# Optimization experiments

Hardware: AMD Instinct MI355X
Metric: run time of the kernel (lower is better)

The kernel has to match this reference:

```python
import jax, jax.numpy as jnp
import numpy as np
from itertools import combinations

N_QUBITS = 8
N_TRASH = 2
N_LAYERS = 4
BATCH = 32768
DIM = 2 ** N_QUBITS  # 256


def _cz_pairs():
    # same CZ pattern as layer() in the torch module; all pairs are distinct,
    # and CZ gates are diagonal and commute, so they fuse into one sign mask.
    pairs = list(combinations(range(N_TRASH), 2))
    for idx in range(N_TRASH):
        for i in range(N_TRASH):
            for j in range(N_TRASH + i, N_QUBITS, N_TRASH):
                pairs.append(((idx + i) % N_TRASH, j))
    return pairs


def _cz_layer_sign():
    bits = np.indices((2,) * N_QUBITS)  # [n_qubits, 2,...,2]; wire 0 = MSB (PennyLane order)
    sign = np.ones((2,) * N_QUBITS, np.float32)
    for a, b in _cz_pairs():
        sign = sign * (1.0 - 2.0 * (bits[a] * bits[b]).astype(np.float32))
    return jnp.asarray(sign)[None]  # broadcast over batch

_CZ_SIGN = _cz_layer_sign()


def _ry(state, theta, w):
    # RY(theta) on wire w, batched over leading axis. state: [B,2,...,2] complex64
    c = jnp.cos(theta / 2).astype(jnp.complex64)
    s = jnp.sin(theta / 2).astype(jnp.complex64)
    g = jnp.stack([jnp.stack([c, -s]), jnp.stack([s, c])])  # [2,2]
    out = jnp.tensordot(g, state, axes=((1,), (1 + w,)))
    return jnp.moveaxis(out, 0, 1 + w)


def _axis_vec(vals, w):
    shape = [1] * (N_QUBITS + 1)
    shape[1 + w] = 2
    return jnp.asarray(vals, dtype=jnp.complex64).reshape(shape)


def _apply_pauli(state, w, p):
    if p == 'X':
        return jnp.flip(state, axis=1 + w)
    if p == 'Y':
        return jnp.flip(state, axis=1 + w) * _axis_vec([-1j, 1j], w)
    return state * _axis_vec([1.0 + 0j, -1.0 + 0j], w)  # Z


def _forward(x, weights):
    # AmplitudeEmbedding(normalize=True)
    norm = jnp.sqrt(jnp.sum(x * x, axis=-1, keepdims=True))
    psi = (x / norm).astype(jnp.complex64).reshape((-1,) + (2,) * N_QUBITS)
    for l in range(N_LAYERS - 1):
        for q in range(N_QUBITS):
            psi = _ry(psi, weights[l * N_QUBITS + q], q)
        psi = psi * _CZ_SIGN  # all CZs of the layer fused into one diagonal
    base = (N_LAYERS - 1) * N_QUBITS
    for q in range(N_TRASH):  # last_layer: RY on trash qubits only
        psi = _ry(psi, weights[base + q], q)

    axes = tuple(range(1, N_QUBITS + 1))
    conj_psi = jnp.conj(psi)

    def ev(op_state):
        return jnp.sum(conj_psi * op_state, axis=axes).real.astype(jnp.float32)

    w0, w1 = 6, 7
    terms = [
        ev(_apply_pauli(psi, w0, 'X')),
        ev(_apply_pauli(psi, w0, 'Y')),
        ev(_apply_pauli(psi, w0, 'Z')),
        ev(_apply_pauli(psi, w1, 'X')),
        ev(_apply_pauli(psi, w1, 'Y')),
        ev(_apply_pauli(psi, w1, 'Z')),
        ev(_apply_pauli(_apply_pauli(psi, w0, 'X'), w1, 'X')),
        ev(_apply_pauli(_apply_pauli(psi, w0, 'Y'), w1, 'Y')),
        ev(_apply_pauli(_apply_pauli(psi, w0, 'Z'), w1, 'Z')),
    ]
    return jnp.stack(terms, axis=1)  # [B, 9]


def setup_inputs() -> dict:
    key = jax.random.key(0)
    kx, kw = jax.random.split(key)
    x = jax.random.normal(kx, (BATCH, DIM), dtype=jnp.float32)
    n_w = N_LAYERS * N_QUBITS - (N_QUBITS - N_TRASH)  # 26
    weights = jax.random.normal(kw, (n_w,), dtype=jnp.float32)
    return {'x': x, 'weights': weights}


def reference(x, weights):
    return _forward(x, weights)
```

## Files before the change

kernel.cpp:

```cpp
#include <hip/hip_runtime.h>
#include <math.h>

#define DIM 256
typedef float v2f __attribute__((ext_vector_type(2)));

__device__ __forceinline__ v2f mk2(float a, float b) { v2f r; r.x = a; r.y = b; return r; }

__device__ __forceinline__ float rl(float v, int l) {
    return __uint_as_float(__builtin_amdgcn_readlane(__float_as_uint(v), l));
}

template<int B2>
__device__ __forceinline__ void ry_pk(v2f* v, float c, float s) {
#pragma unroll
    for (int p = 0; p < 16; ++p)
        if (!(p & (1 << B2))) {
            const int q = p | (1 << B2);
            v2f lo = v[p], hi = v[q];
            v[p] = c * lo - s * hi;
            v[q] = s * lo + c * hi;
        }
}

__device__ __forceinline__ void ry_intra(v2f* v, float c, float s) {
#pragma unroll
    for (int p = 0; p < 16; ++p) {
        float lo = v[p].x, hi = v[p].y;
        v[p].x = fmaf(-s, hi, c * lo);
        v[p].y = fmaf(s, lo, c * hi);
    }
}

__global__ __launch_bounds__(256) void qae_kernel(const float* __restrict__ x,
                                                  const float* __restrict__ w,
                                                  float* __restrict__ out,
                                                  int batch) {
    __shared__ float4 lds4[2048];
    const int lane = threadIdx.x & 63;
    const int wave = blockIdx.x * 4 + (threadIdx.x >> 6);
    const int l3   = lane & 7;
    const int e    = lane >> 3;
    const int eb   = wave * 8 + e;
    float4* W = lds4 + (threadIdx.x >> 6) * 512 + e * 64;

    float h = 0.f;
    if (lane < 20) h = 0.5f * w[lane < 18 ? lane : lane + 4];
    const float cv = __cosf(h), sv = __sinf(h);
#define RYP(B2, slot) ry_pk<B2>(v, rl(cv, slot), rl(sv, slot))
#define RYI(slot)     ry_intra(v, rl(cv, slot), rl(sv, slot))

    const int a0 = (l3 >> 2) & 1, a1 = (l3 >> 1) & 1, a2 = l3 & 1;
    const int aa = a0 & a1, dd = a0 ^ a1;
    const float fE = (aa ^ (dd & a2)) ? -1.f : 1.f;
    const float fO = ((aa ^ (dd & a2)) ^ dd) ? -1.f : 1.f;
    const float pB = (__popc(l3) & 1) ? -1.f : 1.f;
    const v2f mA0 = mk2(fE, fO), mA1 = mk2(fO, fE);
    const v2f mBp = mk2(pB, -pB);

    v2f v[16];
    if (eb < batch) {
        const float* xp = x + (size_t)eb * DIM + l3 * 4;
#pragma unroll
        for (int u = 0; u < 8; ++u) {
            float4 f = *(const float4*)(xp + u * 32);
            v[2 * u]     = mk2(f.x, f.y);
            v[2 * u + 1] = mk2(f.z, f.w);
        }
    } else {
#pragma unroll
        for (int p = 0; p < 16; ++p) v[p] = mk2(0.f, 0.f);
    }
    float nrm2 = 0.f;
#pragma unroll
    for (int p = 0; p < 16; ++p) nrm2 += v[p].x * v[p].x + v[p].y * v[p].y;

    RYP(3, 0); RYP(2, 1); RYP(1, 2);

#pragma unroll
    for (int g = 0; g < 8; ++g)
        W[g * 8 + (l3 ^ g)] = make_float4(v[2*g].x, v[2*g].y, v[2*g+1].x, v[2*g+1].y);
#pragma unroll
    for (int k = 0; k < 8; ++k) {
        float4 f = W[l3 * 8 + (k ^ l3)];
        v[2 * k] = mk2(f.x, f.y); v[2 * k + 1] = mk2(f.z, f.w);
    }

    RYP(3, 3); RYP(2, 4); RYP(1, 5); RYP(0, 6); RYI(7);
#pragma unroll
    for (int p = 0; p < 16; ++p) v[p] *= (__popc(p) & 1) ? mA1 : mA0;
    RYP(3, 11); RYP(2, 12); RYP(1, 13); RYP(0, 14); RYI(15);

#pragma unroll
    for (int k = 0; k < 8; ++k)
        W[l3 * 8 + (k ^ l3)] = make_float4(v[2*k].x, v[2*k].y, v[2*k+1].x, v[2*k+1].y);
#pragma unroll
    for (int g = 0; g < 8; ++g) {
        float4 f = W[g * 8 + (l3 ^ g)];
        v[2 * g] = mk2(f.x, f.y); v[2 * g + 1] = mk2(f.z, f.w);
    }

    RYP(3, 8); RYP(2, 9); RYP(1, 10);
#pragma unroll
    for (int p = 0; p < 16; ++p) {
        const int w0 = (p >> 3) & 1, w1 = (p >> 2) & 1;
        if (w0 & w1)      v[p] = -v[p];
        else if (w0 ^ w1) v[p] *= (__popc(p & 3) & 1) ? -mBp : mBp;
    }
    RYP(3, 16); RYP(2, 17); RYP(0, 18); RYI(19);
#pragma unroll
    for (int p = 0; p < 16; ++p) {
        const int w0 = (p >> 3) & 1, w1 = (p >> 2) & 1;
        if (w0 & w1)      v[p] = -v[p];
        else if (w0 ^ w1) v[p] *= (__popc(p & 3) & 1) ? -mBp : mBp;
    }
#undef RYP
#undef RYI

    float X6 = 0, X7 = 0, XX = 0, YY = 0, Z6 = 0, Z7 = 0, ZZ = 0;
#pragma unroll
    for (int g = 0; g < 8; ++g) {
        float q0 = v[2*g].x, q1 = v[2*g].y, q2 = v[2*g+1].x, q3 = v[2*g+1].y;
        X6 += q0 * q2 + q1 * q3;
        X7 += q0 * q1 + q2 * q3;
        XX += q0 * q3 + q1 * q2;
        YY += q1 * q2 - q0 * q3;
        float s0 = q0*q0, s1 = q1*q1, s2 = q2*q2, s3 = q3*q3;
        Z6 += s0 + s1 - s2 - s3;
        Z7 += s0 - s1 + s2 - s3;
        ZZ += s0 - s1 - s2 + s3;
    }
    X6 *= 2.f; X7 *= 2.f; XX *= 2.f; YY *= 2.f;

#pragma unroll
    for (int m = 1; m < 8; m <<= 1) {
        nrm2 += __shfl_xor(nrm2, m);
        X6 += __shfl_xor(X6, m);  X7 += __shfl_xor(X7, m);
        XX += __shfl_xor(XX, m);  YY += __shfl_xor(YY, m);
        Z6 += __shfl_xor(Z6, m);  Z7 += __shfl_xor(Z7, m);
        ZZ += __shfl_xor(ZZ, m);
    }

    if (eb < batch) {
        const float inv = 1.f / nrm2;
        float* o = out + (size_t)eb * 9;
        const int t = l3;
        if (t < 7) {
            float val = (t == 0) ? X6 : (t == 1) ? Z6 : (t == 2) ? X7
                      : (t == 3) ? Z7 : (t == 4) ? XX : (t == 5) ? YY : ZZ;
            int off = t + (t >= 1 ? 1 : 0) + (t >= 3 ? 1 : 0);
            o[off] = val * inv;
        } else {
            o[1] = 0.f;
            o[4] = 0.f;
        }
    }
}

extern "C" void kernel_launch(void* const* d_in, const int* in_sizes, int n_in,
                              void* d_out, int out_size, void* d_ws, size_t ws_size,
                              hipStream_t stream) {
    const float* x = (const float*)d_in[0];
    const float* w = (const float*)d_in[1];
    float* out = (float*)d_out;
    const int batch = in_sizes[0] / DIM;

    const int waves  = (batch + 7) / 8;
    const int blocks = (waves + 3) / 4;
    qae_kernel<<<blocks, 256, 0, stream>>>(x, w, out, batch);
}
```

Baseline: 79.62 us.

## Split each state vector over 16 lanes with padded scalar LDS transposes

Each batch element's 256-amplitude state is now spread over 16 lanes holding 16 amplitudes each, down from 8 lanes holding 32, so each wave handles 4 elements instead of 8. The qubit-to-lane mapping and gate ordering are rearranged to match, LDS exchanges use padded scalar strides in place of XOR swizzled float4, and the norm is folded into the final reduction. A launch-bounds occupancy hint is added. This cuts register pressure and raises parallelism, at the cost of twice as many waves, more shuffle steps and scalar LDS traffic.

```diff
diff --git a/kernel.cpp b/kernel.cpp
--- a/kernel.cpp
+++ b/kernel.cpp
@@ -13,7 +13,7 @@
 template<int B2>
 __device__ __forceinline__ void ry_pk(v2f* v, float c, float s) {
 #pragma unroll
-    for (int p = 0; p < 16; ++p)
+    for (int p = 0; p < 8; ++p)
         if (!(p & (1 << B2))) {
             const int q = p | (1 << B2);
             v2f lo = v[p], hi = v[q];
@@ -24,24 +24,27 @@
 
 __device__ __forceinline__ void ry_intra(v2f* v, float c, float s) {
 #pragma unroll
-    for (int p = 0; p < 16; ++p) {
+    for (int p = 0; p < 8; ++p) {
         float lo = v[p].x, hi = v[p].y;
         v[p].x = fmaf(-s, hi, c * lo);
         v[p].y = fmaf(s, lo, c * hi);
     }
 }
 
-__global__ __launch_bounds__(256) void qae_kernel(const float* __restrict__ x,
-                                                  const float* __restrict__ w,
-                                                  float* __restrict__ out,
-                                                  int batch) {
-    __shared__ float4 lds4[2048];
+__global__ __launch_bounds__(256, 6) void qae_kernel(const float* __restrict__ x,
+                                                     const float* __restrict__ w,
+                                                     float* __restrict__ out,
+                                                     int batch) {
+    __shared__ float lds[4 * 4 * 272];
     const int lane = threadIdx.x & 63;
-    const int wave = blockIdx.x * 4 + (threadIdx.x >> 6);
-    const int l3   = lane & 7;
-    const int e    = lane >> 3;
-    const int eb   = wave * 8 + e;
-    float4* W = lds4 + (threadIdx.x >> 6) * 512 + e * 64;
+    const int wid  = threadIdx.x >> 6;
+    const int wave = blockIdx.x * 4 + wid;
+    const int nib  = lane & 15;
+    const int e    = lane >> 4;
+    const int eb   = wave * 4 + e;
+    float* WB = lds + wid * 1088 + e * 272;
+    float* pB = WB + nib * 4;
+    float* pA = WB + (nib >> 2) * 68 + (nib & 3);
 
     float h = 0.f;
     if (lane < 20) h = 0.5f * w[lane < 18 ? lane : lane + 4];
@@ -49,91 +52,86 @@
 #define RYP(B2, slot) ry_pk<B2>(v, rl(cv, slot), rl(sv, slot))
 #define RYI(slot)     ry_intra(v, rl(cv, slot), rl(sv, slot))
 
-    const int a0 = (l3 >> 2) & 1, a1 = (l3 >> 1) & 1, a2 = l3 & 1;
-    const int aa = a0 & a1, dd = a0 ^ a1;
-    const float fE = (aa ^ (dd & a2)) ? -1.f : 1.f;
-    const float fO = ((aa ^ (dd & a2)) ^ dd) ? -1.f : 1.f;
-    const float pB = (__popc(l3) & 1) ? -1.f : 1.f;
-    const v2f mA0 = mk2(fE, fO), mA1 = mk2(fO, fE);
-    const v2f mBp = mk2(pB, -pB);
+    float gE, gO;
+    {
+        const int w0 = (nib >> 3) & 1, w1 = (nib >> 2) & 1;
+        const float s0 = (__popc(nib & 3) & 1) ? -1.f : 1.f;
+        if (w0 & w1)      { gE = -1.f; gO = -1.f; }
+        else if (w0 ^ w1) { gE = s0;   gO = -s0;  }
+        else              { gE = 1.f;  gO = 1.f;  }
+    }
+    const v2f mAe = mk2(gE, gO), mAo = mk2(gO, gE);
+    const float pL = (__popc(nib) & 1) ? -1.f : 1.f;
+    const v2f mBx0 = mk2(pL, -pL), mBx1 = mk2(-pL, pL);
 
-    v2f v[16];
+    v2f v[8];
     if (eb < batch) {
-        const float* xp = x + (size_t)eb * DIM + l3 * 4;
+        const float* xp = x + (size_t)eb * DIM + nib * 4;
 #pragma unroll
-        for (int u = 0; u < 8; ++u) {
-            float4 f = *(const float4*)(xp + u * 32);
+        for (int u = 0; u < 4; ++u) {
+            float4 f = *(const float4*)(xp + u * 64);
             v[2 * u]     = mk2(f.x, f.y);
             v[2 * u + 1] = mk2(f.z, f.w);
         }
     } else {
 #pragma unroll
-        for (int p = 0; p < 16; ++p) v[p] = mk2(0.f, 0.f);
+        for (int p = 0; p < 8; ++p) v[p] = mk2(0.f, 0.f);
     }
-    float nrm2 = 0.f;
-#pragma unroll
-    for (int p = 0; p < 16; ++p) nrm2 += v[p].x * v[p].x + v[p].y * v[p].y;
 
-    RYP(3, 0); RYP(2, 1); RYP(1, 2);
+    RYP(2, 0); RYP(1, 1); RYP(0, 6); RYI(7);
 
 #pragma unroll
-    for (int g = 0; g < 8; ++g)
-        W[g * 8 + (l3 ^ g)] = make_float4(v[2*g].x, v[2*g].y, v[2*g+1].x, v[2*g+1].y);
+    for (int u = 0; u < 4; ++u)
+        *(float4*)(pB + u * 68) = make_float4(v[2*u].x, v[2*u].y, v[2*u+1].x, v[2*u+1].y);
 #pragma unroll
-    for (int k = 0; k < 8; ++k) {
-        float4 f = W[l3 * 8 + (k ^ l3)];
-        v[2 * k] = mk2(f.x, f.y); v[2 * k + 1] = mk2(f.z, f.w);
+    for (int p = 0; p < 8; ++p) {
+        v[p].x = pA[p * 8];
+        v[p].y = pA[p * 8 + 4];
     }
 
-    RYP(3, 3); RYP(2, 4); RYP(1, 5); RYP(0, 6); RYI(7);
+    RYP(2, 2); RYP(1, 3); RYP(0, 4); RYI(5);
 #pragma unroll
-    for (int p = 0; p < 16; ++p) v[p] *= (__popc(p) & 1) ? mA1 : mA0;
-    RYP(3, 11); RYP(2, 12); RYP(1, 13); RYP(0, 14); RYI(15);
+    for (int p = 0; p < 8; ++p) v[p] *= (__popc(p) & 1) ? mAo : mAe;
+    RYP(2, 10); RYP(1, 11); RYP(0, 12); RYI(13);
 
 #pragma unroll
-    for (int k = 0; k < 8; ++k)
-        W[l3 * 8 + (k ^ l3)] = make_float4(v[2*k].x, v[2*k].y, v[2*k+1].x, v[2*k+1].y);
+    for (int p = 0; p < 8; ++p) {
+        pA[p * 8]     = v[p].x;
+        pA[p * 8 + 4] = v[p].y;
+    }
 #pragma unroll
-    for (int g = 0; g < 8; ++g) {
-        float4 f = W[g * 8 + (l3 ^ g)];
-        v[2 * g] = mk2(f.x, f.y); v[2 * g + 1] = mk2(f.z, f.w);
+    for (int u = 0; u < 4; ++u) {
+        float4 f = *(const float4*)(pB + u * 68);
+        v[2 * u] = mk2(f.x, f.y); v[2 * u + 1] = mk2(f.z, f.w);
     }
 
-    RYP(3, 8); RYP(2, 9); RYP(1, 10);
-#pragma unroll
-    for (int p = 0; p < 16; ++p) {
-        const int w0 = (p >> 3) & 1, w1 = (p >> 2) & 1;
-        if (w0 & w1)      v[p] = -v[p];
-        else if (w0 ^ w1) v[p] *= (__popc(p & 3) & 1) ? -mBp : mBp;
-    }
-    RYP(3, 16); RYP(2, 17); RYP(0, 18); RYI(19);
-#pragma unroll
-    for (int p = 0; p < 16; ++p) {
-        const int w0 = (p >> 3) & 1, w1 = (p >> 2) & 1;
-        if (w0 & w1)      v[p] = -v[p];
-        else if (w0 ^ w1) v[p] *= (__popc(p & 3) & 1) ? -mBp : mBp;
-    }
+    RYP(2, 8); RYP(1, 9); RYP(0, 14); RYI(15);
+    v[2] *= mBx0; v[3] *= mBx1; v[4] *= mBx0; v[5] *= mBx1; v[6] = -v[6]; v[7] = -v[7];
+    RYP(2, 16); RYP(1, 17); RYP(0, 18); RYI(19);
+    v[2] *= mBx0; v[3] *= mBx1; v[4] *= mBx0; v[5] *= mBx1; v[6] = -v[6]; v[7] = -v[7];
 #undef RYP
 #undef RYI
 
-    float X6 = 0, X7 = 0, XX = 0, YY = 0, Z6 = 0, Z7 = 0, ZZ = 0;
+    float X6 = 0, X7 = 0, XX = 0, YY = 0, Z6 = 0, Z7 = 0, ZZ = 0, N = 0;
 #pragma unroll
-    for (int g = 0; g < 8; ++g) {
-        float q0 = v[2*g].x, q1 = v[2*g].y, q2 = v[2*g+1].x, q3 = v[2*g+1].y;
+    for (int u = 0; u < 4; ++u) {
+        float q0 = v[2*u].x, q1 = v[2*u].y, q2 = v[2*u+1].x, q3 = v[2*u+1].y;
         X6 += q0 * q2 + q1 * q3;
         X7 += q0 * q1 + q2 * q3;
         XX += q0 * q3 + q1 * q2;
         YY += q1 * q2 - q0 * q3;
-        float s0 = q0*q0, s1 = q1*q1, s2 = q2*q2, s3 = q3*q3;
-        Z6 += s0 + s1 - s2 - s3;
-        Z7 += s0 - s1 + s2 - s3;
-        ZZ += s0 - s1 - s2 + s3;
+        float t01p = q0*q0 + q1*q1, t01m = q0*q0 - q1*q1;
+        float t23p = q2*q2 + q3*q3, t23m = q2*q2 - q3*q3;
+        N  += t01p + t23p;
+        Z6 += t01p - t23p;
+        Z7 += t01m + t23m;
+        ZZ += t01m - t23m;
     }
     X6 *= 2.f; X7 *= 2.f; XX *= 2.f; YY *= 2.f;
 
 #pragma unroll
-    for (int m = 1; m < 8; m <<= 1) {
-        nrm2 += __shfl_xor(nrm2, m);
+    for (int m = 1; m < 16; m <<= 1) {
+        N  += __shfl_xor(N, m);
         X6 += __shfl_xor(X6, m);  X7 += __shfl_xor(X7, m);
         XX += __shfl_xor(XX, m);  YY += __shfl_xor(YY, m);
         Z6 += __shfl_xor(Z6, m);  Z7 += __shfl_xor(Z7, m);
@@ -141,15 +139,15 @@
     }
 
     if (eb < batch) {
-        const float inv = 1.f / nrm2;
+        const float inv = 1.f / N;
         float* o = out + (size_t)eb * 9;
-        const int t = l3;
+        const int t = nib;
         if (t < 7) {
             float val = (t == 0) ? X6 : (t == 1) ? Z6 : (t == 2) ? X7
                       : (t == 3) ? Z7 : (t == 4) ? XX : (t == 5) ? YY : ZZ;
             int off = t + (t >= 1 ? 1 : 0) + (t >= 3 ? 1 : 0);
             o[off] = val * inv;
-        } else {
+        } else if (t == 7) {
             o[1] = 0.f;
             o[4] = 0.f;
         }
@@ -164,7 +162,7 @@
     float* out = (float*)d_out;
     const int batch = in_sizes[0] / DIM;
 
-    const int waves  = (batch + 7) / 8;
+    const int waves  = (batch + 3) / 4;
     const int blocks = (waves + 3) / 4;
     qae_kernel<<<blocks, 256, 0, stream>>>(x, w, out, batch);
 }
```

Result: no change. 78.89 us (-0.9%).

## Precompute circuit unitary and apply it via fp16 MFMA GEMM

Applied to the files above, without the earlier changes.

Splits the work into two kernels. The first builds the full 256x256 circuit unitary by simulating the gates on basis vectors and stores it in fp16, in an MFMA-friendly layout, in the workspace. The second multiplies each batch of input states by this unitary with 16x16x32 fp16 MFMA instructions and reduces the Pauli expectations from the accumulators. This replaces per-sample VALU gate simulation with tensor-core matrix multiplication, at the cost of fp16 rounding of inputs and the unitary, plus repeated staging of U into LDS in every block.

```diff
diff --git a/kernel.cpp b/kernel.cpp
--- a/kernel.cpp
+++ b/kernel.cpp
@@ -2,10 +2,11 @@
 #include <math.h>
 
 #define DIM 256
-typedef float v2f __attribute__((ext_vector_type(2)));
+typedef float v2f  __attribute__((ext_vector_type(2)));
+typedef _Float16 f16x8 __attribute__((ext_vector_type(8)));
+typedef float f32x4 __attribute__((ext_vector_type(4)));
 
 __device__ __forceinline__ v2f mk2(float a, float b) { v2f r; r.x = a; r.y = b; return r; }
-
 __device__ __forceinline__ float rl(float v, int l) {
     return __uint_as_float(__builtin_amdgcn_readlane(__float_as_uint(v), l));
 }
@@ -21,7 +22,6 @@
             v[q] = s * lo + c * hi;
         }
 }
-
 __device__ __forceinline__ void ry_intra(v2f* v, float c, float s) {
 #pragma unroll
     for (int p = 0; p < 16; ++p) {
@@ -31,17 +31,16 @@
     }
 }
 
-__global__ __launch_bounds__(256) void qae_kernel(const float* __restrict__ x,
-                                                  const float* __restrict__ w,
-                                                  float* __restrict__ out,
-                                                  int batch) {
+__global__ __launch_bounds__(256) void qae_buildU(const float* __restrict__ w,
+                                                  _Float16* __restrict__ uf) {
     __shared__ float4 lds4[2048];
     const int lane = threadIdx.x & 63;
-    const int wave = blockIdx.x * 4 + (threadIdx.x >> 6);
+    const int wid  = threadIdx.x >> 6;
+    const int wave = blockIdx.x * 4 + wid;
     const int l3   = lane & 7;
     const int e    = lane >> 3;
-    const int eb   = wave * 8 + e;
-    float4* W = lds4 + (threadIdx.x >> 6) * 512 + e * 64;
+    const int col  = wave * 8 + e;
+    float4* W = lds4 + wid * 512 + e * 64;
 
     float h = 0.f;
     if (lane < 20) h = 0.5f * w[lane < 18 ? lane : lane + 4];
@@ -58,101 +57,135 @@
     const v2f mBp = mk2(pB, -pB);
 
     v2f v[16];
-    if (eb < batch) {
-        const float* xp = x + (size_t)eb * DIM + l3 * 4;
-#pragma unroll
-        for (int u = 0; u < 8; ++u) {
-            float4 f = *(const float4*)(xp + u * 32);
-            v[2 * u]     = mk2(f.x, f.y);
-            v[2 * u + 1] = mk2(f.z, f.w);
-        }
-    } else {
-#pragma unroll
-        for (int p = 0; p < 16; ++p) v[p] = mk2(0.f, 0.f);
-    }
-    float nrm2 = 0.f;
-#pragma unroll
-    for (int p = 0; p < 16; ++p) nrm2 += v[p].x * v[p].x + v[p].y * v[p].y;
+#pragma unroll
+    for (int p = 0; p < 16; ++p) v[p] = mk2(0.f, 0.f);
+    if (((col >> 2) & 7) == l3) {
+        const int p = 2 * (col >> 5) + ((col >> 1) & 1);
+        if (col & 1) v[p].y = 1.f; else v[p].x = 1.f;
+    }
 
     RYP(3, 0); RYP(2, 1); RYP(1, 2);
-
 #pragma unroll
     for (int g = 0; g < 8; ++g)
         W[g * 8 + (l3 ^ g)] = make_float4(v[2*g].x, v[2*g].y, v[2*g+1].x, v[2*g+1].y);
 #pragma unroll
     for (int k = 0; k < 8; ++k) {
         float4 f = W[l3 * 8 + (k ^ l3)];
-        v[2 * k] = mk2(f.x, f.y); v[2 * k + 1] = mk2(f.z, f.w);
-    }
-
+        v[2*k] = mk2(f.x, f.y); v[2*k+1] = mk2(f.z, f.w);
+    }
     RYP(3, 3); RYP(2, 4); RYP(1, 5); RYP(0, 6); RYI(7);
 #pragma unroll
     for (int p = 0; p < 16; ++p) v[p] *= (__popc(p) & 1) ? mA1 : mA0;
     RYP(3, 11); RYP(2, 12); RYP(1, 13); RYP(0, 14); RYI(15);
-
 #pragma unroll
     for (int k = 0; k < 8; ++k)
         W[l3 * 8 + (k ^ l3)] = make_float4(v[2*k].x, v[2*k].y, v[2*k+1].x, v[2*k+1].y);
 #pragma unroll
     for (int g = 0; g < 8; ++g) {
         float4 f = W[g * 8 + (l3 ^ g)];
-        v[2 * g] = mk2(f.x, f.y); v[2 * g + 1] = mk2(f.z, f.w);
-    }
-
+        v[2*g] = mk2(f.x, f.y); v[2*g+1] = mk2(f.z, f.w);
+    }
     RYP(3, 8); RYP(2, 9); RYP(1, 10);
 #pragma unroll
     for (int p = 0; p < 16; ++p) {
-        const int w0 = (p >> 3) & 1, w1 = (p >> 2) & 1;
-        if (w0 & w1)      v[p] = -v[p];
-        else if (w0 ^ w1) v[p] *= (__popc(p & 3) & 1) ? -mBp : mBp;
+        const int b0 = (p >> 3) & 1, b1 = (p >> 2) & 1;
+        if (b0 & b1)      v[p] = -v[p];
+        else if (b0 ^ b1) v[p] *= (__popc(p & 3) & 1) ? -mBp : mBp;
     }
     RYP(3, 16); RYP(2, 17); RYP(0, 18); RYI(19);
 #pragma unroll
     for (int p = 0; p < 16; ++p) {
-        const int w0 = (p >> 3) & 1, w1 = (p >> 2) & 1;
-        if (w0 & w1)      v[p] = -v[p];
-        else if (w0 ^ w1) v[p] *= (__popc(p & 3) & 1) ? -mBp : mBp;
+        const int b0 = (p >> 3) & 1, b1 = (p >> 2) & 1;
+        if (b0 & b1)      v[p] = -v[p];
+        else if (b0 ^ b1) v[p] *= (__popc(p & 3) & 1) ? -mBp : mBp;
     }
 #undef RYP
 #undef RYI
 
-    float X6 = 0, X7 = 0, XX = 0, YY = 0, Z6 = 0, Z7 = 0, ZZ = 0;
-#pragma unroll
-    for (int g = 0; g < 8; ++g) {
-        float q0 = v[2*g].x, q1 = v[2*g].y, q2 = v[2*g+1].x, q3 = v[2*g+1].y;
-        X6 += q0 * q2 + q1 * q3;
-        X7 += q0 * q1 + q2 * q3;
-        XX += q0 * q3 + q1 * q2;
-        YY += q1 * q2 - q0 * q3;
-        float s0 = q0*q0, s1 = q1*q1, s2 = q2*q2, s3 = q3*q3;
-        Z6 += s0 + s1 - s2 - s3;
-        Z7 += s0 - s1 + s2 - s3;
-        ZZ += s0 - s1 - s2 + s3;
-    }
-    X6 *= 2.f; X7 *= 2.f; XX *= 2.f; YY *= 2.f;
-
-#pragma unroll
-    for (int m = 1; m < 8; m <<= 1) {
-        nrm2 += __shfl_xor(nrm2, m);
-        X6 += __shfl_xor(X6, m);  X7 += __shfl_xor(X7, m);
-        XX += __shfl_xor(XX, m);  YY += __shfl_xor(YY, m);
-        Z6 += __shfl_xor(Z6, m);  Z7 += __shfl_xor(Z7, m);
-        ZZ += __shfl_xor(ZZ, m);
-    }
-
-    if (eb < batch) {
-        const float inv = 1.f / nrm2;
-        float* o = out + (size_t)eb * 9;
-        const int t = l3;
-        if (t < 7) {
-            float val = (t == 0) ? X6 : (t == 1) ? Z6 : (t == 2) ? X7
-                      : (t == 3) ? Z7 : (t == 4) ? XX : (t == 5) ? YY : ZZ;
-            int off = t + (t >= 1 ? 1 : 0) + (t >= 3 ? 1 : 0);
-            o[off] = val * inv;
-        } else {
-            o[1] = 0.f;
-            o[4] = 0.f;
+    const int ks = col >> 5, j = col & 7, lfhi = ((col >> 3) & 3) << 4;
+#pragma unroll
+    for (int p = 0; p < 16; ++p) {
+        const int mbase = ((p >> 1) << 5) | (l3 << 2) | ((p & 1) << 1);
+        {   const int m = mbase, mt = m >> 4, lf = (m & 15) | lfhi;
+            uf[(size_t)(((mt * 8 + ks) * 64 + lf) * 8 + j)] = (_Float16)v[p].x; }
+        {   const int m = mbase | 1, mt = m >> 4, lf = (m & 15) | lfhi;
+            uf[(size_t)(((mt * 8 + ks) * 64 + lf) * 8 + j)] = (_Float16)v[p].y; }
+    }
+}
+
+__global__ __launch_bounds__(256) void qae_gemm(const float* __restrict__ x,
+                                                const _Float16* __restrict__ uf,
+                                                float* __restrict__ out, int batch) {
+    __shared__ __align__(16) _Float16 Ut[16384];
+    const int lane  = threadIdx.x & 63;
+    const int wid   = threadIdx.x >> 6;
+    const int strip = blockIdx.x * 4 + wid;
+    const int bl = lane & 15, bq = lane >> 4;
+    const int b  = strip * 16 + bl;
+    const bool act = (b < batch);
+
+    const float* xp = x + (size_t)b * DIM + bq * 8;
+    f16x8 bf[8];
+    float nrm = 0.f;
+#pragma unroll
+    for (int ks = 0; ks < 8; ++ks) {
+        float4 f0 = make_float4(0.f, 0.f, 0.f, 0.f), f1 = f0;
+        if (act) { f0 = *(const float4*)(xp + 32 * ks);
+                   f1 = *(const float4*)(xp + 32 * ks + 4); }
+        nrm += f0.x*f0.x + f0.y*f0.y + f0.z*f0.z + f0.w*f0.w
+             + f1.x*f1.x + f1.y*f1.y + f1.z*f1.z + f1.w*f1.w;
+        bf[ks][0] = (_Float16)f0.x; bf[ks][1] = (_Float16)f0.y;
+        bf[ks][2] = (_Float16)f0.z; bf[ks][3] = (_Float16)f0.w;
+        bf[ks][4] = (_Float16)f1.x; bf[ks][5] = (_Float16)f1.y;
+        bf[ks][6] = (_Float16)f1.z; bf[ks][7] = (_Float16)f1.w;
+    }
+
+    float pX6 = 0, pX7 = 0, pXX = 0, pYY = 0, pZ6 = 0, pZ7 = 0, pZZ = 0;
+
+#pragma unroll
+    for (int ph = 0; ph < 4; ++ph) {
+        __syncthreads();
+        const float4* src = (const float4*)uf + (size_t)ph * 2048 + threadIdx.x;
+        float4* dst = (float4*)Ut;
+#pragma unroll
+        for (int i = 0; i < 8; ++i)
+            dst[i * 256 + threadIdx.x] = src[i * 256];
+        __syncthreads();
+#pragma unroll
+        for (int mtl = 0; mtl < 4; ++mtl) {
+            f32x4 acc = {0.f, 0.f, 0.f, 0.f};
+#pragma unroll
+            for (int ks = 0; ks < 8; ++ks) {
+                f16x8 af = *(const f16x8*)(Ut + ((mtl * 8 + ks) * 64 + lane) * 8);
+                acc = __builtin_amdgcn_mfma_f32_16x16x32_f16(af, bf[ks], acc, 0, 0, 0);
+            }
+            const float q0 = acc[0], q1 = acc[1], q2 = acc[2], q3 = acc[3];
+            pX6 += q0 * q2 + q1 * q3;
+            pX7 += q0 * q1 + q2 * q3;
+            pXX += q0 * q3 + q1 * q2;
+            pYY += q1 * q2 - q0 * q3;
+            const float s0 = q0*q0, s1 = q1*q1, s2 = q2*q2, s3 = q3*q3;
+            pZ6 += (s0 + s1) - (s2 + s3);
+            pZ7 += (s0 - s1) + (s2 - s3);
+            pZZ += (s0 - s1) - (s2 - s3);
         }
+    }
+
+#pragma unroll
+    for (int m = 16; m <= 32; m <<= 1) {
+        nrm += __shfl_xor(nrm, m);
+        pX6 += __shfl_xor(pX6, m); pX7 += __shfl_xor(pX7, m);
+        pXX += __shfl_xor(pXX, m); pYY += __shfl_xor(pYY, m);
+        pZ6 += __shfl_xor(pZ6, m); pZ7 += __shfl_xor(pZ7, m);
+        pZZ += __shfl_xor(pZZ, m);
+    }
+
+    if (act && bq == 0) {
+        const float inv = 1.f / nrm;
+        float* o = out + (size_t)b * 9;
+        o[0] = 2.f * pX6 * inv;  o[1] = 0.f;  o[2] = pZ6 * inv;
+        o[3] = 2.f * pX7 * inv;  o[4] = 0.f;  o[5] = pZ7 * inv;
+        o[6] = 2.f * pXX * inv;  o[7] = 2.f * pYY * inv;  o[8] = pZZ * inv;
     }
 }
 
@@ -162,9 +195,11 @@
     const float* x = (const float*)d_in[0];
     const float* w = (const float*)d_in[1];
     float* out = (float*)d_out;
+    _Float16* uf = (_Float16*)d_ws;
     const int batch = in_sizes[0] / DIM;
 
-    const int waves  = (batch + 7) / 8;
-    const int blocks = (waves + 3) / 4;
-    qae_kernel<<<blocks, 256, 0, stream>>>(x, w, out, batch);
-}
+    qae_buildU<<<8, 256, 0, stream>>>(w, uf);
+
+    const int strips = (batch + 15) / 16;
+    qae_gemm<<<(strips + 3) / 4, 256, 0, stream>>>(x, uf, out, batch);
+}
```

After: 92.63 us. 1.16x slower.
